# Performance work log

Hardware: AMD Instinct MI355X
Metric: run time of the kernel (lower is better)

Reference implementation:

```python
import jax, jax.numpy as jnp
import numpy as np

WS = 8          # cubic window size (D_sp = H_sp = W_sp)
SS = 4          # shift size per axis (WS // 2)
NH = 12         # num heads
HD = 32         # head dim = 4*feature_size // num_head
SCALE = HD ** -0.5
N = WS ** 3     # tokens per window = 512


def _rel_index():
    # static relative-position index, computed once in numpy
    c = np.stack(np.meshgrid(np.arange(WS), np.arange(WS), np.arange(WS), indexing='ij')).reshape(3, -1)
    r = (c[:, :, None] - c[:, None, :]).transpose(1, 2, 0)  # [N, N, 3]
    r[:, :, 0] += WS - 1
    r[:, :, 1] += WS - 1
    r[:, :, 2] += WS - 1
    r[:, :, 0] *= (2 * WS - 1) ** 2
    r[:, :, 1] *= (2 * WS - 1)
    return r.sum(-1)  # [N, N] int


def _shift_mask(Dp, Hp, Wp):
    # static shifted-window attention mask, computed once in numpy
    img = np.zeros((Dp, Hp, Wp))
    sl = lambda w, s: (slice(None, -w), slice(-w, -s), slice(-s, None))
    cnt = 0
    for d in sl(WS, SS):
        for h in sl(WS, SS):
            for w in sl(WS, SS):
                img[d, h, w] = cnt
                cnt += 1
    mw = img.reshape(Dp // WS, WS, Hp // WS, WS, Wp // WS, WS).transpose(0, 2, 4, 1, 3, 5).reshape(-1, N)
    am = mw[:, None, :] - mw[:, :, None]  # [nw, N, N]
    return np.where(am != 0, -100.0, 0.0).astype(np.float32)


_REL_IDX = _rel_index()


def setup_inputs() -> dict:
    key = jax.random.key(0)
    k1, k2 = jax.random.split(key)
    qkv = jax.random.normal(k1, (1, 32, 32, 32, 1152), dtype=jnp.float32)
    bias_table = jax.random.normal(k2, ((2 * WS - 1) ** 3, NH), dtype=jnp.float32) * 0.02
    return {"qkv": qkv, "bias_table": bias_table}


def reference(qkv, bias_table):
    B, D, H, W, C = qkv.shape
    pd = (WS - D % WS) % WS
    ph = (WS - H % WS) % WS
    pw = (WS - W % WS) % WS
    qkv = jnp.pad(qkv, ((0, 0), (0, pd), (0, ph), (0, pw), (0, 0)))
    _, Dp, Hp, Wp, _ = qkv.shape
    # shift
    qkv = jnp.roll(qkv, (-SS, -SS, -SS), axis=(1, 2, 3))
    Cq = C // 3
    qkv = qkv.reshape(B, Dp, Hp, Wp, 3, Cq).transpose(4, 0, 1, 2, 3, 5)  # [3,B,Dp,Hp,Wp,Cq]

    def part(x):  # window partition -> [num_windows*B, NH, N, HD]
        x = x.reshape(B, Dp // WS, WS, Hp // WS, WS, Wp // WS, WS, HD, NH)
        return x.transpose(0, 1, 3, 5, 8, 2, 4, 6, 7).reshape(-1, NH, N, HD)

    q, k, v = part(qkv[0]), part(qkv[1]), part(qkv[2])
    attn = jnp.einsum('whnd,whmd->whnm', q * SCALE, k)  # [W*B, NH, N, N]
    bias = bias_table[_REL_IDX.reshape(-1)].reshape(N, N, NH).transpose(2, 0, 1)  # [NH,N,N]
    attn = attn + bias[None]
    mask = jnp.asarray(_shift_mask(Dp, Hp, Wp))  # [nw, N, N]
    nw = mask.shape[0]
    attn = attn.reshape(B, nw, NH, N, N) + mask[None, :, None]
    attn = jax.nn.softmax(attn.reshape(-1, NH, N, N), axis=-1)
    x = jnp.einsum('whnm,whmd->whnd', attn, v)  # [W*B, NH, N, HD]
    # merge heads exactly as torch: permute(0,2,3,1) -> channels = (HD, NH)
    x = x.transpose(0, 2, 3, 1).reshape(-1, N, Cq)
    # window reverse
    x = x.reshape(-1, Dp // WS, Hp // WS, Wp // WS, WS, WS, WS, Cq)
    x = x.transpose(0, 1, 4, 2, 5, 3, 6, 7).reshape(-1, Dp, Hp, Wp, Cq)
    x = jnp.roll(x, (SS, SS, SS), axis=(1, 2, 3))
    return x[:, :D, :H, :W, :]
```

## Files before the change

### kernel.cpp

```cpp
#include <hip/hip_runtime.h>
#include <hip/hip_bf16.h>


typedef __attribute__((ext_vector_type(8))) short short8_t;
typedef __attribute__((ext_vector_type(4))) float f32x4;

__device__ float g_biasC[12 * 32 * 16 * 64 * 8];
__device__ uint4 g_pack4[3ULL * 12 * 64 * 512 * 32 / 8];
__device__ unsigned short g_opack[12ULL * 64 * 32 * 512];

constexpr float SCL2E = 0.17677669529663687f * 1.4426950408889634f;
constexpr float LOG2E = 1.4426950408889634f;

__device__ __forceinline__ unsigned short f2bf(float f) {
  __hip_bfloat16 h = __float2bfloat16(f);
  return *reinterpret_cast<unsigned short*>(&h);
}
__device__ __forceinline__ unsigned pkbf2(float lo, float hi) {
  __hip_bfloat162 h2 = __float22bfloat162_rn(make_float2(lo, hi));
  return *reinterpret_cast<unsigned*>(&h2);
}

__global__ __launch_bounds__(256, 4) void prep_kernel(
    const float* __restrict__ qkv, const float* __restrict__ table) {
  __shared__ unsigned short S[8 * 1154];
  const int bid = blockIdx.x;
  const int tid = threadIdx.x;

  if (bid >= 4096) {
    int flat = (bid - 4096) * 256 + tid;
    int l  = flat & 63;
    int c  = (flat >> 6) & 15;
    int qt = (flat >> 10) & 31;
    int nh = flat >> 15;
    int ln = l & 15, g = l >> 4;
    int n = qt * 16 + ln;
    int dn = n >> 6, hn = (n >> 3) & 7, wn = n & 7;
    float e[8];
#pragma unroll
    for (int r = 0; r < 8; ++r) {
      int m = 32 * c + (r >> 2) * 16 + g * 4 + (r & 3);
      int dm = m >> 6, hm = (m >> 3) & 7, wm = m & 7;
      int idx = (dn - dm + 7) * 225 + (hn - hm + 7) * 15 + (wn - wm + 7);
      e[r] = table[idx * 12 + nh] * LOG2E;
    }
    *(float4*)&g_biasC[flat * 8]     = make_float4(e[0], e[1], e[2], e[3]);
    *(float4*)&g_biasC[flat * 8 + 4] = make_float4(e[4], e[5], e[6], e[7]);
    return;
  }

  const int mh = bid & 7;
  const int md = (bid >> 3) & 7;
  const int w = bid >> 6;
  const int dblk = w >> 4, hblk = (w >> 2) & 3, wblk = w & 3;
  const int dd = (dblk * 8 + 4 + md) & 31;
  const int hh = (hblk * 8 + 4 + mh) & 31;
  const int w0 = wblk * 8 + 4;

#pragma unroll
  for (int rep = 0; rep < 9; ++rep) {
    int t = rep * 256 + tid;
    unsigned v = (unsigned)t / 288u;
    int c4 = t - (int)v * 288;
    int ww = (w0 + (int)v) & 31;
    float4 f = *(const float4*)(qkv + (((dd * 32 + hh) * 32 + ww) * 1152) + c4 * 4);
    if (c4 < 96) {
      f.x *= SCL2E; f.y *= SCL2E; f.z *= SCL2E; f.w *= SCL2E;
    }
    *(uint2*)&S[v * 1154 + c4 * 4] = make_uint2(pkbf2(f.x, f.y), pkbf2(f.z, f.w));
  }
  __syncthreads();

  const int mbase = md * 64 + mh * 8;
  unsigned short* gp = (unsigned short*)g_pack4;
#pragma unroll
  for (int rep = 0; rep < 5; ++rep) {
    int t = rep * 256 + tid;
    if (t < 1152) {
      int chunk = t & 3;
      int mw = (t >> 2) & 7;
      int r = t >> 5;
      int nh = r % 12;
      int part = r / 12;
      int ebase = mw * 1154 + part * 384 + chunk * 96 + nh;
      unsigned pk[4];
#pragma unroll
      for (int jj = 0; jj < 4; ++jj) {
        unsigned lo = S[ebase + (2 * jj) * 12];
        unsigned hi = S[ebase + (2 * jj + 1) * 12];
        pk[jj] = lo | (hi << 16);
      }
      size_t dst = ((((size_t)(part * 12 + nh) * 64 + w) * 512 + mbase + mw) * 32 + chunk * 8);
      *(uint4*)&gp[dst] = make_uint4(pk[0], pk[1], pk[2], pk[3]);
    }
  }
}

__global__ __launch_bounds__(512, 4) void swin_attn_kernel() {
  __shared__ __align__(16) unsigned short Klds[512 * 32];
  __shared__ __align__(16) unsigned short Vt[32 * 516];

  const int bid = blockIdx.x;
  const int xcd = bid & 7;
  const int jb = bid >> 3;
  int nh, w;
  if (jb < 64) { nh = xcd; w = jb; }
  else         { nh = 8 + (xcd >> 1); w = (xcd & 1) * 32 + (jb - 64); }
  const int dblk = w >> 4, hblk = (w >> 2) & 3, wblk = w & 3;
  const int bm = ((dblk == 3) ? 256 : 0) | ((hblk == 3) ? 32 : 0) |
                 ((wblk == 3) ? 4 : 0);

  const int tid = threadIdx.x;

  const unsigned short* gp = (const unsigned short*)g_pack4;
  const size_t base = ((size_t)nh * 64 + w) * (512 * 32);
  const unsigned short* Qg = gp + base;
  const unsigned short* Kg = gp + (size_t)1 * 12 * 64 * 512 * 32 + base;
  const unsigned short* Vg = gp + (size_t)2 * 12 * 64 * 512 * 32 + base;

#pragma unroll
  for (int itr = 0; itr < 4; ++itr) {
    int flat = itr * 512 + tid;
    int m = flat >> 2, chunk = flat & 3;
    uint4 d = *(const uint4*)(Kg + flat * 8);
    char* dst = (char*)Klds + m * 64 + ((chunk * 16) ^ ((m & 3) << 4));
    *(uint4*)dst = d;
  }
#pragma unroll
  for (int itr = 0; itr < 4; ++itr) {
    int flat = itr * 512 + tid;
    int m = flat >> 2, hc = flat & 3;
    uint4 d = *(const uint4*)(Vg + flat * 8);
    const unsigned u[4] = {d.x, d.y, d.z, d.w};
#pragma unroll
    for (int jj = 0; jj < 8; ++jj) {
      Vt[(hc * 8 + jj) * 516 + m] =
          (unsigned short)((u[jj >> 1] >> (16 * (jj & 1))) & 0xffffu);
    }
  }
  __syncthreads();

  const int l = tid & 63;
  const int wv = tid >> 6;
  const int ln = l & 15;
  const int g = l >> 4;

  union frag { unsigned u[4]; short8_t v; };

  frag qf[4];
#pragma unroll
  for (int it = 0; it < 4; ++it) {
    const int n = (wv * 4 + it) * 16 + ln;
    const uint4 qd = *(const uint4*)(Qg + n * 32 + g * 8);
    qf[it].u[0] = qd.x; qf[it].u[1] = qd.y; qf[it].u[2] = qd.z; qf[it].u[3] = qd.w;
  }
  f32x4 o0[4], o1[4], sumac[4];
#pragma unroll
  for (int it = 0; it < 4; ++it) {
    o0[it] = (f32x4)(0.0f); o1[it] = (f32x4)(0.0f); sumac[it] = (f32x4)(0.0f);
  }
  frag ones;
  ones.u[0] = 0x3F803F80u; ones.u[1] = 0x3F803F80u;
  ones.u[2] = 0x3F803F80u; ones.u[3] = 0x3F803F80u;

  const f32x4* bp = (const f32x4*)g_biasC +
      ((size_t)(nh * 32 + wv * 4) * 16) * 128 + l * 2;

  int nA[4];
#pragma unroll
  for (int it = 0; it < 4; ++it) nA[it] = ((wv * 4 + it) * 16 + ln) & bm;

#define CLOOP(MASKED)                                                          \
  _Pragma("unroll 1")                                                          \
  for (int c = 0; c < 16; ++c) {                                               \
    frag k0, k1, a0, a1;                                                       \
    k0.v = *(const short8_t*)((const char*)Klds +                              \
        (((2 * c) * 16 + ln) * 64 + ((g * 16) ^ ((ln & 3) << 4))));            \
    k1.v = *(const short8_t*)((const char*)Klds +                              \
        (((2 * c + 1) * 16 + ln) * 64 + ((g * 16) ^ ((ln & 3) << 4))));        \
    {                                                                          \
      const int col = c * 32 + g * 4;                                          \
      const unsigned* v00 = (const unsigned*)&Vt[ln * 516 + col];              \
      const unsigned* v01 = (const unsigned*)&Vt[ln * 516 + col + 16];         \
      a0.u[0] = v00[0]; a0.u[1] = v00[1]; a0.u[2] = v01[0]; a0.u[3] = v01[1];  \
      const unsigned* v10 = (const unsigned*)&Vt[(16 + ln) * 516 + col];       \
      const unsigned* v11 = (const unsigned*)&Vt[(16 + ln) * 516 + col + 16];  \
      a1.u[0] = v10[0]; a1.u[1] = v10[1]; a1.u[2] = v11[0]; a1.u[3] = v11[1];  \
    }                                                                          \
    const int mAnd = ((c << 5) | ((g & 1) << 2)) & bm;                         \
    _Pragma("unroll")                                                          \
    for (int it = 0; it < 4; ++it) {                                           \
      const f32x4 bc0 = bp[(it * 16 + c) * 128];                               \
      const f32x4 bc1 = bp[(it * 16 + c) * 128 + 1];                           \
      f32x4 acc0 = __builtin_amdgcn_mfma_f32_16x16x32_bf16(                    \
          k0.v, qf[it].v, bc0, 0, 0, 0);                                       \
      f32x4 acc1 = __builtin_amdgcn_mfma_f32_16x16x32_bf16(                    \
          k1.v, qf[it].v, bc1, 0, 0, 0);                                       \
      float p0 = __builtin_amdgcn_exp2f(acc0[0]);                              \
      float p1 = __builtin_amdgcn_exp2f(acc0[1]);                              \
      float p2 = __builtin_amdgcn_exp2f(acc0[2]);                              \
      float p3 = __builtin_amdgcn_exp2f(acc0[3]);                              \
      float p4 = __builtin_amdgcn_exp2f(acc1[0]);                              \
      float p5 = __builtin_amdgcn_exp2f(acc1[1]);                              \
      float p6 = __builtin_amdgcn_exp2f(acc1[2]);                              \
      float p7 = __builtin_amdgcn_exp2f(acc1[3]);                              \
      frag pf;                                                                 \
      pf.u[0] = pkbf2(p0, p1);  pf.u[1] = pkbf2(p2, p3);                       \
      pf.u[2] = pkbf2(p4, p5);  pf.u[3] = pkbf2(p6, p7);                       \
      if (MASKED) {                                                            \
        const bool keep = (nA[it] == mAnd);                                    \
        pf.u[0] = keep ? pf.u[0] : 0u;                                         \
        pf.u[1] = keep ? pf.u[1] : 0u;                                         \
        pf.u[2] = keep ? pf.u[2] : 0u;                                         \
        pf.u[3] = keep ? pf.u[3] : 0u;                                         \
      }                                                                        \
      sumac[it] = __builtin_amdgcn_mfma_f32_16x16x32_bf16(                     \
          ones.v, pf.v, sumac[it], 0, 0, 0);                                   \
      o0[it] = __builtin_amdgcn_mfma_f32_16x16x32_bf16(a0.v, pf.v, o0[it], 0, 0, 0); \
      o1[it] = __builtin_amdgcn_mfma_f32_16x16x32_bf16(a1.v, pf.v, o1[it], 0, 0, 0); \
    }                                                                          \
  }

  if (bm == 0) { CLOOP(false) } else { CLOOP(true) }
#undef CLOOP

#pragma unroll
  for (int it = 0; it < 4; ++it) {
    const float rinv = 1.0f / sumac[it][0];
    const int qt = wv * 4 + it;
    unsigned short* gop = g_opack + ((size_t)nh * 64 + w) * 16384 + qt * 512 + ln;
#pragma unroll
    for (int r = 0; r < 4; ++r) {
      gop[(g * 4 + r) * 16] = f2bf(o0[it][r] * rinv);
      gop[(g * 4 + r + 16) * 16] = f2bf(o1[it][r] * rinv);
    }
  }
}

__global__ __launch_bounds__(256) void unpack_kernel(float* __restrict__ out) {
  __shared__ float S[32 * 388];
  const int bid = blockIdx.x;
  const int mc = bid & 15;
  const int w = bid >> 4;
  const int dblk = w >> 4, hblk = (w >> 2) & 3, wblk = w & 3;
  const int d0 = dblk * 8 + 4, h0 = hblk * 8 + 4, w0 = wblk * 8 + 4;
  const int tid = threadIdx.x;

#pragma unroll
  for (int rep = 0; rep < 6; ++rep) {
    int task = rep * 256 + tid;
    int tk8 = task & 1;
    int q2 = (task >> 1) & 1;
    int hd = (task >> 2) & 31;
    int nh = task >> 7;
    const uint4 d = *(const uint4*)(g_opack +
        ((size_t)nh * 64 + w) * 16384 + (size_t)(mc * 2 + q2) * 512 + hd * 16 + tk8 * 8);
    const unsigned u[4] = {d.x, d.y, d.z, d.w};
#pragma unroll
    for (int jj = 0; jj < 8; ++jj) {
      unsigned bits = (u[jj >> 1] << (16 * (1 - (jj & 1)))) & 0xffff0000u;
      S[(q2 * 16 + tk8 * 8 + jj) * 388 + hd * 12 + nh] = __uint_as_float(bits);
    }
  }
  __syncthreads();

#pragma unroll
  for (int rep = 0; rep < 12; ++rep) {
    int task = rep * 256 + tid;
    unsigned c4 = (unsigned)task % 96u;
    int ml = (int)((unsigned)task / 96u);
    int n = mc * 32 + ml;
    int dd = (d0 + (n >> 6)) & 31;
    int hh = (h0 + ((n >> 3) & 7)) & 31;
    int ww = (w0 + (n & 7)) & 31;
    const float4* src = (const float4*)&S[ml * 388 + c4 * 4];
    *(float4*)(out + ((size_t)((dd * 32 + hh) * 32 + ww)) * 384 + c4 * 4) = *src;
  }
}

extern "C" void kernel_launch(void* const* d_in, const int* in_sizes, int n_in,
                              void* d_out, int out_size, void* d_ws, size_t ws_size,
                              hipStream_t stream) {
  (void)in_sizes; (void)n_in; (void)out_size; (void)d_ws; (void)ws_size;
  const float* qkv = (const float*)d_in[0];
  const float* bias_table = (const float*)d_in[1];
  float* out = (float*)d_out;

  prep_kernel<<<5632, 256, 0, stream>>>(qkv, bias_table);
  swin_attn_kernel<<<768, 512, 0, stream>>>();
  unpack_kernel<<<1024, 256, 0, stream>>>(out);
}
```

Baseline: 119.2 us.

## Pre-swizzle K and pre-transpose V in prep kernel, batch loads, raise MFMA priority

The prep kernel now writes K already XOR-swizzled and V already transposed into an hd-major layout, so the attention kernel can copy both into LDS with wide vector stores. This replaces the per-element 16-bit scatter used to transpose V in LDS. Global loads in both kernels are issued in a batch before any use, so more memory requests are in flight at once. The MFMA section is wrapped in s_setprio to favour matrix waves. The cost is more registers for the load buffers and a more complex write pattern in the prep kernel.

```diff
diff --git a/kernel.cpp b/kernel.cpp
--- a/kernel.cpp
+++ b/kernel.cpp
@@ -57,16 +57,23 @@
   const int hh = (hblk * 8 + 4 + mh) & 31;
   const int w0 = wblk * 8 + 4;
 
+  float4 buf[9];
 #pragma unroll
   for (int rep = 0; rep < 9; ++rep) {
     int t = rep * 256 + tid;
     unsigned v = (unsigned)t / 288u;
     int c4 = t - (int)v * 288;
     int ww = (w0 + (int)v) & 31;
-    float4 f = *(const float4*)(qkv + (((dd * 32 + hh) * 32 + ww) * 1152) + c4 * 4);
-    if (c4 < 96) {
-      f.x *= SCL2E; f.y *= SCL2E; f.z *= SCL2E; f.w *= SCL2E;
-    }
+    buf[rep] = *(const float4*)(qkv + (((dd * 32 + hh) * 32 + ww) * 1152) + c4 * 4);
+  }
+#pragma unroll
+  for (int rep = 0; rep < 9; ++rep) {
+    int t = rep * 256 + tid;
+    unsigned v = (unsigned)t / 288u;
+    int c4 = t - (int)v * 288;
+    float4 f = buf[rep];
+    const float sc = (c4 < 96) ? SCL2E : 1.0f;
+    f.x *= sc; f.y *= sc; f.z *= sc; f.w *= sc;
     *(uint2*)&S[v * 1154 + c4 * 4] = make_uint2(pkbf2(f.x, f.y), pkbf2(f.z, f.w));
   }
   __syncthreads();
@@ -77,20 +84,36 @@
   for (int rep = 0; rep < 5; ++rep) {
     int t = rep * 256 + tid;
     if (t < 1152) {
-      int chunk = t & 3;
-      int mw = (t >> 2) & 7;
       int r = t >> 5;
       int nh = r % 12;
       int part = r / 12;
-      int ebase = mw * 1154 + part * 384 + chunk * 96 + nh;
       unsigned pk[4];
-#pragma unroll
-      for (int jj = 0; jj < 4; ++jj) {
-        unsigned lo = S[ebase + (2 * jj) * 12];
-        unsigned hi = S[ebase + (2 * jj + 1) * 12];
-        pk[jj] = lo | (hi << 16);
+      size_t dst;
+      if (part < 2) {
+        int chunk = t & 3;
+        int mw = (t >> 2) & 7;
+        int ebase = mw * 1154 + part * 384 + chunk * 96 + nh;
+#pragma unroll
+        for (int jj = 0; jj < 4; ++jj) {
+          unsigned lo = S[ebase + (2 * jj) * 12];
+          unsigned hi = S[ebase + (2 * jj + 1) * 12];
+          pk[jj] = lo | (hi << 16);
+        }
+        int m = mbase + mw;
+        int off = (part == 0) ? (m * 32 + chunk * 8)
+                              : (m * 32 + ((chunk * 8) ^ ((mw & 3) << 3)));
+        dst = ((size_t)(part * 12 + nh) * 64 + w) * 16384 + off;
+      } else {
+        int hd = t & 31;
+        int ebase = 768 + hd * 12 + nh;
+#pragma unroll
+        for (int jj = 0; jj < 4; ++jj) {
+          unsigned lo = S[(2 * jj) * 1154 + ebase];
+          unsigned hi = S[(2 * jj + 1) * 1154 + ebase];
+          pk[jj] = lo | (hi << 16);
+        }
+        dst = ((size_t)(24 + nh) * 64 + w) * 16384 + (md * 8 + mh) * 256 + hd * 8;
       }
-      size_t dst = ((((size_t)(part * 12 + nh) * 64 + w) * 512 + mbase + mw) * 32 + chunk * 8);
       *(uint4*)&gp[dst] = make_uint4(pk[0], pk[1], pk[2], pk[3]);
     }
   }
@@ -118,25 +141,20 @@
   const unsigned short* Kg = gp + (size_t)1 * 12 * 64 * 512 * 32 + base;
   const unsigned short* Vg = gp + (size_t)2 * 12 * 64 * 512 * 32 + base;
 
+  uint4 kb[4], vb[4];
+#pragma unroll
+  for (int itr = 0; itr < 4; ++itr) kb[itr] = *(const uint4*)(Kg + (itr * 512 + tid) * 8);
+#pragma unroll
+  for (int itr = 0; itr < 4; ++itr) vb[itr] = *(const uint4*)(Vg + (itr * 512 + tid) * 8);
+#pragma unroll
+  for (int itr = 0; itr < 4; ++itr)
+    *(uint4*)((char*)Klds + (itr * 512 + tid) * 16) = kb[itr];
 #pragma unroll
   for (int itr = 0; itr < 4; ++itr) {
     int flat = itr * 512 + tid;
-    int m = flat >> 2, chunk = flat & 3;
-    uint4 d = *(const uint4*)(Kg + flat * 8);
-    char* dst = (char*)Klds + m * 64 + ((chunk * 16) ^ ((m & 3) << 4));
-    *(uint4*)dst = d;
-  }
-#pragma unroll
-  for (int itr = 0; itr < 4; ++itr) {
-    int flat = itr * 512 + tid;
-    int m = flat >> 2, hc = flat & 3;
-    uint4 d = *(const uint4*)(Vg + flat * 8);
-    const unsigned u[4] = {d.x, d.y, d.z, d.w};
-#pragma unroll
-    for (int jj = 0; jj < 8; ++jj) {
-      Vt[(hc * 8 + jj) * 516 + m] =
-          (unsigned short)((u[jj >> 1] >> (16 * (jj & 1))) & 0xffffu);
-    }
+    int hd = flat & 31, mb8 = flat >> 5;
+    *(uint2*)&Vt[hd * 516 + mb8 * 8]     = make_uint2(vb[itr].x, vb[itr].y);
+    *(uint2*)&Vt[hd * 516 + mb8 * 8 + 4] = make_uint2(vb[itr].z, vb[itr].w);
   }
   __syncthreads();
 
@@ -188,6 +206,7 @@
       a1.u[0] = v10[0]; a1.u[1] = v10[1]; a1.u[2] = v11[0]; a1.u[3] = v11[1];  \
     }                                                                          \
     const int mAnd = ((c << 5) | ((g & 1) << 2)) & bm;                         \
+    __builtin_amdgcn_s_setprio(1);                                             \
     _Pragma("unroll")                                                          \
     for (int it = 0; it < 4; ++it) {                                           \
       const f32x4 bc0 = bp[(it * 16 + c) * 128];                               \
@@ -219,6 +238,7 @@
       o0[it] = __builtin_amdgcn_mfma_f32_16x16x32_bf16(a0.v, pf.v, o0[it], 0, 0, 0); \
       o1[it] = __builtin_amdgcn_mfma_f32_16x16x32_bf16(a1.v, pf.v, o1[it], 0, 0, 0); \
     }                                                                          \
+    __builtin_amdgcn_s_setprio(0);                                             \
   }
 
   if (bm == 0) { CLOOP(false) } else { CLOOP(true) }
```

Result: no change. 121.4 us (+1.8%).
